# Optimization experiments

Hardware: AMD Instinct MI355X
Metric: run time of the kernel (lower is better)

The kernel has to match this reference:

```python
import jax, jax.numpy as jnp
import numpy as np

N = 100000
E = 1600000
D = 64
BETA = 1.0


def setup_inputs() -> dict:
    key = jax.random.key(0)
    ks = jax.random.split(key, 6)
    x = jax.random.normal(ks[0], (N, D), dtype=jnp.float32)
    edge_index = jax.random.randint(ks[1], (2, E), 0, N, dtype=jnp.int64)
    s = 1.0 / np.sqrt(D)
    Wm = jax.random.uniform(ks[2], (D, D), jnp.float32, -s, s)
    bm = jax.random.uniform(ks[3], (D,), jnp.float32, -s, s)
    Wr = jax.random.uniform(ks[4], (D, D), jnp.float32, -s, s)
    br = jax.random.uniform(ks[5], (D,), jnp.float32, -s, s)
    return {"x": x, "edge_index": edge_index, "Wm": Wm, "bm": bm, "Wr": Wr, "br": br}


def reference(x, edge_index, Wm, bm, Wr, br):
    row, col = edge_index[0], edge_index[1]
    # gather source features and apply message linear: [E, D]
    messages = x[row] @ Wm + bm
    scores = BETA * messages.mean(axis=-1)  # [E]
    # edge softmax over incoming edges of each destination node (col)
    seg_max = jax.ops.segment_max(scores, col, num_segments=N)  # [N]
    ex = jnp.exp(scores - seg_max[col])  # [E]
    seg_sum = jax.ops.segment_sum(ex, col, num_segments=N)  # [N]
    weights = ex / seg_sum[col]  # [E]
    # weighted scatter-add back to destinations
    out = jax.ops.segment_sum(messages * weights[:, None], col, num_segments=N)
    return out + (x @ Wr + br)
```

## Files before the change

kernel.cpp:

```cpp
#include <hip/hip_runtime.h>
#include <math.h>

#define N_NODES 100000
#define DIM 64
#define N_EDGES 1600000

#define NBF 1563
#define BK_NODES 64
#define CAP 1408

#define SC_CHUNK 8192
#define SC_BLOCKS ((N_EDGES + SC_CHUNK - 1) / SC_CHUNK)

#define GEMM_BLOCKS ((N_NODES / 16 + 15) / 16)
#define PH_BLOCKS (SC_BLOCKS + GEMM_BLOCKS)

typedef _Float16 half8 __attribute__((ext_vector_type(8)));
typedef _Float16 half4 __attribute__((ext_vector_type(4)));
typedef float f32x4 __attribute__((ext_vector_type(4)));

__global__ __launch_bounds__(1024) void k_phase(
        const float* __restrict__ x,
        const float* __restrict__ Wm, const float* __restrict__ bm,
        const float* __restrict__ Wr, const float* __restrict__ br,
        const int* __restrict__ row, const int* __restrict__ col,
        int* __restrict__ cursor, unsigned int* __restrict__ pairs,
        _Float16* __restrict__ Mh, float* __restrict__ es,
        float* __restrict__ out) {
    __shared__ int cnt[NBF];
    __shared__ int base_l[NBF];
    __shared__ int wsum[16];
    __shared__ int segtot;
    __shared__ unsigned int stage[SC_CHUNK];
    __shared__ unsigned short stage_bk[SC_CHUNK];

    const int t = threadIdx.x;
    const int lane = t & 63;
    const int wid = t >> 6;

    if (blockIdx.x < SC_BLOCKS) {
        const int start = blockIdx.x * SC_CHUNK;
        const int mEnd = min(N_EDGES, start + SC_CHUNK);

        for (int i = t; i < NBF; i += 1024) cnt[i] = 0;
        __syncthreads();

        int rr[8], cc[8], lr[8];
#pragma unroll
        for (int k = 0; k < 8; ++k) {
            const int idx = start + k * 1024 + t;
            if (idx < mEnd) {
                cc[k] = col[idx];
                rr[k] = row[idx];
                lr[k] = atomicAdd(&cnt[cc[k] >> 6], 1);
            }
        }
        __syncthreads();

        int segbase = 0;
        for (int s = 0; s < NBF; s += 1024) {
            const int i = s + t;
            const int v = (i < NBF) ? cnt[i] : 0;
            int inc = v;
#pragma unroll
            for (int o = 1; o < 64; o <<= 1) {
                const int u = __shfl_up(inc, o, 64);
                if (lane >= o) inc += u;
            }
            if (lane == 63) wsum[wid] = inc;
            __syncthreads();
            if (wid == 0) {
                const int wv = (lane < 16) ? wsum[lane] : 0;
                int winc = wv;
#pragma unroll
                for (int o = 1; o < 16; o <<= 1) {
                    const int u = __shfl_up(winc, o, 64);
                    if (lane >= o) winc += u;
                }
                if (lane < 16) wsum[lane] = winc - wv;
            }
            __syncthreads();
            const int excl = segbase + inc - v + wsum[wid];
            if (i < NBF) {
                base_l[i] = excl;
                if (v > 0) cnt[i] = atomicAdd(&cursor[i], v) - excl;
            }
            if (t == 1023) segtot = excl + v;
            __syncthreads();
            segbase = segtot;
        }

#pragma unroll
        for (int k = 0; k < 8; ++k) {
            const int idx = start + k * 1024 + t;
            if (idx < mEnd) {
                const int bk = cc[k] >> 6;
                const int slot = base_l[bk] + lr[k];
                stage[slot] = ((unsigned int)rr[k] << 6) | (unsigned int)(cc[k] & 63);
                stage_bk[slot] = (unsigned short)bk;
            }
        }
        __syncthreads();

        const int m = mEnd - start;
        for (int i = t; i < m; i += 1024) {
            const int bk = stage_bk[i];
            const int gslot = cnt[bk] + i;
            if (gslot < CAP) pairs[(size_t)bk * CAP + gslot] = stage[i];
        }
        return;
    }

    const int wave = (blockIdx.x - SC_BLOCKS) * 16 + wid;
    if (wave >= N_NODES / 16) return;
    const int quad = lane >> 4;
    const int l15 = lane & 15;
    const int row0 = wave * 16;

    half8 bfrag[8][2];
#pragma unroll
    for (int ct = 0; ct < 8; ++ct) {
        const float* W = (ct < 4) ? Wm : Wr;
        const int c = (ct & 3) * 16 + l15;
#pragma unroll
        for (int kc = 0; kc < 2; ++kc) {
            half8 f;
#pragma unroll
            for (int j = 0; j < 8; ++j)
                f[j] = (_Float16)W[(kc * 32 + quad * 8 + j) * DIM + c];
            bfrag[ct][kc] = f;
        }
    }

    half8 afrag[2];
#pragma unroll
    for (int kc = 0; kc < 2; ++kc) {
        const float* xp = x + (size_t)(row0 + l15) * DIM + kc * 32 + quad * 8;
        const float4 x0 = *(const float4*)xp;
        const float4 x1 = *(const float4*)(xp + 4);
        half8 f;
        f[0] = (_Float16)x0.x; f[1] = (_Float16)x0.y;
        f[2] = (_Float16)x0.z; f[3] = (_Float16)x0.w;
        f[4] = (_Float16)x1.x; f[5] = (_Float16)x1.y;
        f[6] = (_Float16)x1.z; f[7] = (_Float16)x1.w;
        afrag[kc] = f;
    }

    f32x4 acc[8];
#pragma unroll
    for (int ct = 0; ct < 8; ++ct) {
        f32x4 a = {0.f, 0.f, 0.f, 0.f};
        a = __builtin_amdgcn_mfma_f32_16x16x32_f16(afrag[0], bfrag[ct][0], a, 0, 0, 0);
        a = __builtin_amdgcn_mfma_f32_16x16x32_f16(afrag[1], bfrag[ct][1], a, 0, 0, 0);
        acc[ct] = a;
    }

    float rsum[4] = {0.f, 0.f, 0.f, 0.f};
#pragma unroll
    for (int ct = 0; ct < 8; ++ct) {
        const float bias = (ct < 4) ? bm[(ct & 3) * 16 + l15]
                                    : br[(ct & 3) * 16 + l15];
#pragma unroll
        for (int r = 0; r < 4; ++r) {
            const float v = acc[ct][r] + bias;
            const size_t idx = (size_t)(row0 + quad * 4 + r) * DIM + (ct & 3) * 16 + l15;
            if (ct < 4) {
                Mh[idx] = (_Float16)v;
                rsum[r] += v;
            } else {
                out[idx] = v;
            }
        }
    }
#pragma unroll
    for (int o = 1; o <= 8; o <<= 1) {
#pragma unroll
        for (int r = 0; r < 4; ++r) rsum[r] += __shfl_xor(rsum[r], o, 64);
    }
    if (l15 == 0) {
#pragma unroll
        for (int r = 0; r < 4; ++r)
            es[row0 + quad * 4 + r] = __expf(rsum[r] * (1.0f / DIM));
    }
}

__global__ __launch_bounds__(512) void k_bucket_gather(
        const unsigned int* __restrict__ pairs, const int* __restrict__ cursor,
        const float* __restrict__ es, const half4* __restrict__ Mh4,
        float4* __restrict__ out4) {
    __shared__ unsigned int sorted[CAP];
    __shared__ int cnt[BK_NODES];
    __shared__ int off[BK_NODES];
    const int b = blockIdx.x;
    const int t = threadIdx.x;
    const int lane = t & 63;
    const int wid = t >> 6;
    const int m = min(cursor[b], CAP);
    const size_t base = (size_t)b * CAP;

    if (t < BK_NODES) cnt[t] = 0;
    __syncthreads();

    unsigned int pk[3];
    int rk[3];
#pragma unroll
    for (int k = 0; k < 3; ++k) {
        const int i = k * 512 + t;
        if (i < m) {
            pk[k] = pairs[base + i];
            rk[k] = atomicAdd(&cnt[pk[k] & 63u], 1);
        }
    }
    __syncthreads();

    if (wid == 0) {
        const int v = cnt[lane];
        int inc = v;
#pragma unroll
        for (int o = 1; o < 64; o <<= 1) {
            const int u = __shfl_up(inc, o, 64);
            if (lane >= o) inc += u;
        }
        off[lane] = inc - v;
    }
    __syncthreads();

#pragma unroll
    for (int k = 0; k < 3; ++k) {
        const int i = k * 512 + t;
        if (i < m) sorted[off[pk[k] & 63u] + rk[k]] = pk[k];
    }
    __syncthreads();

    const int g = t >> 4;
    const int gl = t & 15;
    for (int c = g; c < BK_NODES; c += 32) {
        const int node = b * BK_NODES + c;
        if (node >= N_NODES) break;
        const int s0i = off[c];
        const int len = cnt[c];
        if (len == 0) continue;

        float a0x = 0.f, a0y = 0.f, a0z = 0.f, a0w = 0.f, l0 = 0.f;
        float a1x = 0.f, a1y = 0.f, a1z = 0.f, a1w = 0.f, l1 = 0.f;
        float a2x = 0.f, a2y = 0.f, a2z = 0.f, a2w = 0.f, l2 = 0.f;
        float a3x = 0.f, a3y = 0.f, a3z = 0.f, a3w = 0.f, l3 = 0.f;
        int j = 0;
        for (; j + 3 < len; j += 4) {
            const int s0 = (int)(sorted[s0i + j] >> 6);
            const int s1 = (int)(sorted[s0i + j + 1] >> 6);
            const int s2 = (int)(sorted[s0i + j + 2] >> 6);
            const int s3 = (int)(sorted[s0i + j + 3] >> 6);
            const float w0 = es[s0];
            const float w1 = es[s1];
            const float w2 = es[s2];
            const float w3 = es[s3];
            const half4 m0 = Mh4[(size_t)s0 * 16 + gl];
            const half4 m1 = Mh4[(size_t)s1 * 16 + gl];
            const half4 m2 = Mh4[(size_t)s2 * 16 + gl];
            const half4 m3 = Mh4[(size_t)s3 * 16 + gl];
            l0 += w0; l1 += w1; l2 += w2; l3 += w3;
            a0x = fmaf(w0, (float)m0[0], a0x); a0y = fmaf(w0, (float)m0[1], a0y);
            a0z = fmaf(w0, (float)m0[2], a0z); a0w = fmaf(w0, (float)m0[3], a0w);
            a1x = fmaf(w1, (float)m1[0], a1x); a1y = fmaf(w1, (float)m1[1], a1y);
            a1z = fmaf(w1, (float)m1[2], a1z); a1w = fmaf(w1, (float)m1[3], a1w);
            a2x = fmaf(w2, (float)m2[0], a2x); a2y = fmaf(w2, (float)m2[1], a2y);
            a2z = fmaf(w2, (float)m2[2], a2z); a2w = fmaf(w2, (float)m2[3], a2w);
            a3x = fmaf(w3, (float)m3[0], a3x); a3y = fmaf(w3, (float)m3[1], a3y);
            a3z = fmaf(w3, (float)m3[2], a3z); a3w = fmaf(w3, (float)m3[3], a3w);
        }
        for (; j < len; ++j) {
            const int s0 = (int)(sorted[s0i + j] >> 6);
            const float w0 = es[s0];
            const half4 m0 = Mh4[(size_t)s0 * 16 + gl];
            l0 += w0;
            a0x = fmaf(w0, (float)m0[0], a0x); a0y = fmaf(w0, (float)m0[1], a0y);
            a0z = fmaf(w0, (float)m0[2], a0z); a0w = fmaf(w0, (float)m0[3], a0w);
        }
        const float inv = 1.0f / (l0 + l1 + l2 + l3);
        float4 r = out4[(size_t)node * 16 + gl];
        r.x = fmaf(a0x + a1x + a2x + a3x, inv, r.x);
        r.y = fmaf(a0y + a1y + a2y + a3y, inv, r.y);
        r.z = fmaf(a0z + a1z + a2z + a3z, inv, r.z);
        r.w = fmaf(a0w + a1w + a2w + a3w, inv, r.w);
        out4[(size_t)node * 16 + gl] = r;
    }
}

extern "C" void kernel_launch(void* const* d_in, const int* in_sizes, int n_in,
                              void* d_out, int out_size, void* d_ws, size_t ws_size,
                              hipStream_t stream) {
    const float* x  = (const float*)d_in[0];
    const int*   ei = (const int*)d_in[1];
    const float* Wm = (const float*)d_in[2];
    const float* bm = (const float*)d_in[3];
    const float* Wr = (const float*)d_in[4];
    const float* br = (const float*)d_in[5];
    float* out = (float*)d_out;
    const int* row = ei;
    const int* col = ei + N_EDGES;

    char* ws = (char*)d_ws;
    _Float16* Mh    = (_Float16*)ws;     ws += (size_t)N_NODES * DIM * sizeof(_Float16);
    float* es       = (float*)ws;        ws += (size_t)N_NODES * sizeof(float);
    int* cursor     = (int*)ws;          ws += (size_t)2048 * sizeof(int);
    unsigned int* pairs = (unsigned int*)ws; ws += (size_t)NBF * CAP * sizeof(unsigned int);

    hipMemsetAsync(cursor, 0, NBF * sizeof(int), stream);

    k_phase<<<PH_BLOCKS, 1024, 0, stream>>>(x, Wm, bm, Wr, br, row, col,
                                            cursor, pairs, Mh, es, out);
    k_bucket_gather<<<NBF, 512, 0, stream>>>(pairs, cursor, es,
                                             (const half4*)Mh, (float4*)out);
}
```

Baseline: 153.4 us.

## Pre-transpose weights to fp16 in prep kernel and scatter edge pairs directly

Adds a single-block prep kernel that zeroes the bucket cursors (replacing the memset) and writes a transposed fp16 copy of Wm and Wr, so each GEMM wave loads its B fragments as vector half8 loads instead of strided scalar float loads with conversion. The scatter phase drops its block-local prefix scan and shared-memory staging. Each block now reserves global bucket offsets with one atomic per bucket and writes edge pairs straight to global memory. This cuts shared memory use and barriers, which may raise occupancy, but the global writes become less coalesced and an extra kernel launch is added.

```diff
diff --git a/kernel.cpp b/kernel.cpp
--- a/kernel.cpp
+++ b/kernel.cpp
@@ -19,20 +19,31 @@
 typedef _Float16 half4 __attribute__((ext_vector_type(4)));
 typedef float f32x4 __attribute__((ext_vector_type(4)));
 
+__global__ __launch_bounds__(1024) void k_prep(
+        const float* __restrict__ Wm, const float* __restrict__ Wr,
+        _Float16* __restrict__ Wt, int* __restrict__ cursor) {
+    const int t = threadIdx.x;
+    for (int i = t; i < NBF; i += 1024) cursor[i] = 0;
+#pragma unroll
+    for (int k = 0; k < 8; ++k) {
+        const int i = k * 1024 + t;
+        const int c = i >> 6;
+        const int kk = i & 63;
+        const float v = (c < 64) ? Wm[kk * 64 + c] : Wr[kk * 64 + (c - 64)];
+        Wt[i] = (_Float16)v;
+    }
+}
+
 __global__ __launch_bounds__(1024) void k_phase(
         const float* __restrict__ x,
-        const float* __restrict__ Wm, const float* __restrict__ bm,
-        const float* __restrict__ Wr, const float* __restrict__ br,
+        const _Float16* __restrict__ Wt,
+        const float* __restrict__ bm, const float* __restrict__ br,
         const int* __restrict__ row, const int* __restrict__ col,
         int* __restrict__ cursor, unsigned int* __restrict__ pairs,
         _Float16* __restrict__ Mh, float* __restrict__ es,
         float* __restrict__ out) {
     __shared__ int cnt[NBF];
-    __shared__ int base_l[NBF];
-    __shared__ int wsum[16];
-    __shared__ int segtot;
-    __shared__ unsigned int stage[SC_CHUNK];
-    __shared__ unsigned short stage_bk[SC_CHUNK];
+    __shared__ int basg[NBF];
 
     const int t = threadIdx.x;
     const int lane = t & 63;
@@ -57,56 +68,22 @@
         }
         __syncthreads();
 
-        int segbase = 0;
-        for (int s = 0; s < NBF; s += 1024) {
-            const int i = s + t;
-            const int v = (i < NBF) ? cnt[i] : 0;
-            int inc = v;
-#pragma unroll
-            for (int o = 1; o < 64; o <<= 1) {
-                const int u = __shfl_up(inc, o, 64);
-                if (lane >= o) inc += u;
-            }
-            if (lane == 63) wsum[wid] = inc;
-            __syncthreads();
-            if (wid == 0) {
-                const int wv = (lane < 16) ? wsum[lane] : 0;
-                int winc = wv;
-#pragma unroll
-                for (int o = 1; o < 16; o <<= 1) {
-                    const int u = __shfl_up(winc, o, 64);
-                    if (lane >= o) winc += u;
-                }
-                if (lane < 16) wsum[lane] = winc - wv;
-            }
-            __syncthreads();
-            const int excl = segbase + inc - v + wsum[wid];
-            if (i < NBF) {
-                base_l[i] = excl;
-                if (v > 0) cnt[i] = atomicAdd(&cursor[i], v) - excl;
-            }
-            if (t == 1023) segtot = excl + v;
-            __syncthreads();
-            segbase = segtot;
-        }
+        for (int i = t; i < NBF; i += 1024) {
+            const int v = cnt[i];
+            if (v > 0) basg[i] = atomicAdd(&cursor[i], v);
+        }
+        __syncthreads();
 
 #pragma unroll
         for (int k = 0; k < 8; ++k) {
             const int idx = start + k * 1024 + t;
             if (idx < mEnd) {
                 const int bk = cc[k] >> 6;
-                const int slot = base_l[bk] + lr[k];
-                stage[slot] = ((unsigned int)rr[k] << 6) | (unsigned int)(cc[k] & 63);
-                stage_bk[slot] = (unsigned short)bk;
+                const int gslot = basg[bk] + lr[k];
+                if (gslot < CAP)
+                    pairs[(size_t)bk * CAP + gslot] =
+                        ((unsigned int)rr[k] << 6) | (unsigned int)(cc[k] & 63);
             }
-        }
-        __syncthreads();
-
-        const int m = mEnd - start;
-        for (int i = t; i < m; i += 1024) {
-            const int bk = stage_bk[i];
-            const int gslot = cnt[bk] + i;
-            if (gslot < CAP) pairs[(size_t)bk * CAP + gslot] = stage[i];
         }
         return;
     }
@@ -117,19 +94,14 @@
     const int l15 = lane & 15;
     const int row0 = wave * 16;
 
+    const half8* __restrict__ Wt8 = (const half8*)Wt;
     half8 bfrag[8][2];
 #pragma unroll
     for (int ct = 0; ct < 8; ++ct) {
-        const float* W = (ct < 4) ? Wm : Wr;
-        const int c = (ct & 3) * 16 + l15;
-#pragma unroll
-        for (int kc = 0; kc < 2; ++kc) {
-            half8 f;
-#pragma unroll
-            for (int j = 0; j < 8; ++j)
-                f[j] = (_Float16)W[(kc * 32 + quad * 8 + j) * DIM + c];
-            bfrag[ct][kc] = f;
-        }
+        const int cidx = ((ct < 4) ? 0 : 64) + (ct & 3) * 16 + l15;
+#pragma unroll
+        for (int kc = 0; kc < 2; ++kc)
+            bfrag[ct][kc] = Wt8[cidx * 8 + kc * 4 + quad];
     }
 
     half8 afrag[2];
@@ -304,11 +276,11 @@
     _Float16* Mh    = (_Float16*)ws;     ws += (size_t)N_NODES * DIM * sizeof(_Float16);
     float* es       = (float*)ws;        ws += (size_t)N_NODES * sizeof(float);
     int* cursor     = (int*)ws;          ws += (size_t)2048 * sizeof(int);
+    _Float16* Wt    = (_Float16*)ws;     ws += (size_t)128 * 64 * sizeof(_Float16);
     unsigned int* pairs = (unsigned int*)ws; ws += (size_t)NBF * CAP * sizeof(unsigned int);
 
-    hipMemsetAsync(cursor, 0, NBF * sizeof(int), stream);
-
-    k_phase<<<PH_BLOCKS, 1024, 0, stream>>>(x, Wm, bm, Wr, br, row, col,
+    k_prep<<<1, 1024, 0, stream>>>(Wm, Wr, Wt, cursor);
+    k_phase<<<PH_BLOCKS, 1024, 0, stream>>>(x, Wt, bm, br, row, col,
                                             cursor, pairs, Mh, es, out);
     k_bucket_gather<<<NBF, 512, 0, stream>>>(pairs, cursor, es,
                                              (const half4*)Mh, (float4*)out);
```

After: 167.1 us. +8.9%, slower.

## Zero bucket cursors in-kernel behind a spin flag; gather with half8 per lane

Applied to the files above, without the earlier changes.

The host memset of the bucket cursors is removed. Block 0 of the phase kernel now zeroes them and publishes a magic flag, and every scatter block spin-waits on that flag before it takes its bucket cursor offsets. The gather kernel switches from 16 lanes per node with half4 loads to 8 lanes per node with half8 loads, so all 64 nodes of a bucket are handled at once without an inner node loop. Costs and risks: the flag is never reset, so on repeated calls the wait may no longer order the zeroing ahead of the cursor atomics. The spin also relies on block 0 being resident.

```diff
diff --git a/kernel.cpp b/kernel.cpp
--- a/kernel.cpp
+++ b/kernel.cpp
@@ -8,6 +8,9 @@
 #define NBF 1563
 #define BK_NODES 64
 #define CAP 1408
+
+#define CFLAG 2047
+#define CMAGIC 0x1357ACE9
 
 #define SC_CHUNK 8192
 #define SC_BLOCKS ((N_EDGES + SC_CHUNK - 1) / SC_CHUNK)
@@ -39,6 +42,15 @@
     const int wid = t >> 6;
 
     if (blockIdx.x < SC_BLOCKS) {
+        if (blockIdx.x == 0) {
+            for (int i = t; i < NBF; i += 1024) atomicExch(&cursor[i], 0);
+            __syncthreads();
+            if (t == 0) {
+                __threadfence();
+                atomicExch(&cursor[CFLAG], CMAGIC);
+            }
+        }
+
         const int start = blockIdx.x * SC_CHUNK;
         const int mEnd = min(N_EDGES, start + SC_CHUNK);
 
@@ -54,6 +66,11 @@
                 rr[k] = row[idx];
                 lr[k] = atomicAdd(&cnt[cc[k] >> 6], 1);
             }
+        }
+        __syncthreads();
+
+        if (t == 0) {
+            while (atomicAdd(&cursor[CFLAG], 0) != CMAGIC) {}
         }
         __syncthreads();
 
@@ -186,7 +203,7 @@
 
 __global__ __launch_bounds__(512) void k_bucket_gather(
         const unsigned int* __restrict__ pairs, const int* __restrict__ cursor,
-        const float* __restrict__ es, const half4* __restrict__ Mh4,
+        const float* __restrict__ es, const half8* __restrict__ Mh8,
         float4* __restrict__ out4) {
     __shared__ unsigned int sorted[CAP];
     __shared__ int cnt[BK_NODES];
@@ -232,59 +249,64 @@
     }
     __syncthreads();
 
-    const int g = t >> 4;
-    const int gl = t & 15;
-    for (int c = g; c < BK_NODES; c += 32) {
-        const int node = b * BK_NODES + c;
-        if (node >= N_NODES) break;
-        const int s0i = off[c];
-        const int len = cnt[c];
-        if (len == 0) continue;
-
-        float a0x = 0.f, a0y = 0.f, a0z = 0.f, a0w = 0.f, l0 = 0.f;
-        float a1x = 0.f, a1y = 0.f, a1z = 0.f, a1w = 0.f, l1 = 0.f;
-        float a2x = 0.f, a2y = 0.f, a2z = 0.f, a2w = 0.f, l2 = 0.f;
-        float a3x = 0.f, a3y = 0.f, a3z = 0.f, a3w = 0.f, l3 = 0.f;
-        int j = 0;
-        for (; j + 3 < len; j += 4) {
-            const int s0 = (int)(sorted[s0i + j] >> 6);
-            const int s1 = (int)(sorted[s0i + j + 1] >> 6);
-            const int s2 = (int)(sorted[s0i + j + 2] >> 6);
-            const int s3 = (int)(sorted[s0i + j + 3] >> 6);
-            const float w0 = es[s0];
-            const float w1 = es[s1];
-            const float w2 = es[s2];
-            const float w3 = es[s3];
-            const half4 m0 = Mh4[(size_t)s0 * 16 + gl];
-            const half4 m1 = Mh4[(size_t)s1 * 16 + gl];
-            const half4 m2 = Mh4[(size_t)s2 * 16 + gl];
-            const half4 m3 = Mh4[(size_t)s3 * 16 + gl];
-            l0 += w0; l1 += w1; l2 += w2; l3 += w3;
-            a0x = fmaf(w0, (float)m0[0], a0x); a0y = fmaf(w0, (float)m0[1], a0y);
-            a0z = fmaf(w0, (float)m0[2], a0z); a0w = fmaf(w0, (float)m0[3], a0w);
-            a1x = fmaf(w1, (float)m1[0], a1x); a1y = fmaf(w1, (float)m1[1], a1y);
-            a1z = fmaf(w1, (float)m1[2], a1z); a1w = fmaf(w1, (float)m1[3], a1w);
-            a2x = fmaf(w2, (float)m2[0], a2x); a2y = fmaf(w2, (float)m2[1], a2y);
-            a2z = fmaf(w2, (float)m2[2], a2z); a2w = fmaf(w2, (float)m2[3], a2w);
-            a3x = fmaf(w3, (float)m3[0], a3x); a3y = fmaf(w3, (float)m3[1], a3y);
-            a3z = fmaf(w3, (float)m3[2], a3z); a3w = fmaf(w3, (float)m3[3], a3w);
-        }
-        for (; j < len; ++j) {
-            const int s0 = (int)(sorted[s0i + j] >> 6);
-            const float w0 = es[s0];
-            const half4 m0 = Mh4[(size_t)s0 * 16 + gl];
-            l0 += w0;
-            a0x = fmaf(w0, (float)m0[0], a0x); a0y = fmaf(w0, (float)m0[1], a0y);
-            a0z = fmaf(w0, (float)m0[2], a0z); a0w = fmaf(w0, (float)m0[3], a0w);
-        }
-        const float inv = 1.0f / (l0 + l1 + l2 + l3);
-        float4 r = out4[(size_t)node * 16 + gl];
-        r.x = fmaf(a0x + a1x + a2x + a3x, inv, r.x);
-        r.y = fmaf(a0y + a1y + a2y + a3y, inv, r.y);
-        r.z = fmaf(a0z + a1z + a2z + a3z, inv, r.z);
-        r.w = fmaf(a0w + a1w + a2w + a3w, inv, r.w);
-        out4[(size_t)node * 16 + gl] = r;
-    }
+    const int g = t >> 3;
+    const int gl = t & 7;
+    const int node = b * BK_NODES + g;
+    if (node >= N_NODES) return;
+    const int s0i = off[g];
+    const int len = cnt[g];
+    if (len == 0) return;
+
+    float a0[8], a1[8], a2[8], a3[8];
+    float l0 = 0.f, l1 = 0.f, l2 = 0.f, l3 = 0.f;
+#pragma unroll
+    for (int d = 0; d < 8; ++d) { a0[d] = 0.f; a1[d] = 0.f; a2[d] = 0.f; a3[d] = 0.f; }
+
+    int j = 0;
+    for (; j + 3 < len; j += 4) {
+        const int s0 = (int)(sorted[s0i + j] >> 6);
+        const int s1 = (int)(sorted[s0i + j + 1] >> 6);
+        const int s2 = (int)(sorted[s0i + j + 2] >> 6);
+        const int s3 = (int)(sorted[s0i + j + 3] >> 6);
+        const float w0 = es[s0];
+        const float w1 = es[s1];
+        const float w2 = es[s2];
+        const float w3 = es[s3];
+        const half8 m0 = Mh8[(size_t)s0 * 8 + gl];
+        const half8 m1 = Mh8[(size_t)s1 * 8 + gl];
+        const half8 m2 = Mh8[(size_t)s2 * 8 + gl];
+        const half8 m3 = Mh8[(size_t)s3 * 8 + gl];
+        l0 += w0; l1 += w1; l2 += w2; l3 += w3;
+#pragma unroll
+        for (int d = 0; d < 8; ++d) {
+            a0[d] = fmaf(w0, (float)m0[d], a0[d]);
+            a1[d] = fmaf(w1, (float)m1[d], a1[d]);
+            a2[d] = fmaf(w2, (float)m2[d], a2[d]);
+            a3[d] = fmaf(w3, (float)m3[d], a3[d]);
+        }
+    }
+    for (; j < len; ++j) {
+        const int s0 = (int)(sorted[s0i + j] >> 6);
+        const float w0 = es[s0];
+        const half8 m0 = Mh8[(size_t)s0 * 8 + gl];
+        l0 += w0;
+#pragma unroll
+        for (int d = 0; d < 8; ++d) a0[d] = fmaf(w0, (float)m0[d], a0[d]);
+    }
+
+    const float inv = 1.0f / (l0 + l1 + l2 + l3);
+    float4 r0 = out4[(size_t)node * 16 + gl * 2];
+    float4 r1 = out4[(size_t)node * 16 + gl * 2 + 1];
+    r0.x = fmaf(a0[0] + a1[0] + a2[0] + a3[0], inv, r0.x);
+    r0.y = fmaf(a0[1] + a1[1] + a2[1] + a3[1], inv, r0.y);
+    r0.z = fmaf(a0[2] + a1[2] + a2[2] + a3[2], inv, r0.z);
+    r0.w = fmaf(a0[3] + a1[3] + a2[3] + a3[3], inv, r0.w);
+    r1.x = fmaf(a0[4] + a1[4] + a2[4] + a3[4], inv, r1.x);
+    r1.y = fmaf(a0[5] + a1[5] + a2[5] + a3[5], inv, r1.y);
+    r1.z = fmaf(a0[6] + a1[6] + a2[6] + a3[6], inv, r1.z);
+    r1.w = fmaf(a0[7] + a1[7] + a2[7] + a3[7], inv, r1.w);
+    out4[(size_t)node * 16 + gl * 2] = r0;
+    out4[(size_t)node * 16 + gl * 2 + 1] = r1;
 }
 
 extern "C" void kernel_launch(void* const* d_in, const int* in_sizes, int n_in,
@@ -306,10 +328,8 @@
     int* cursor     = (int*)ws;          ws += (size_t)2048 * sizeof(int);
     unsigned int* pairs = (unsigned int*)ws; ws += (size_t)NBF * CAP * sizeof(unsigned int);
 
-    hipMemsetAsync(cursor, 0, NBF * sizeof(int), stream);
-
     k_phase<<<PH_BLOCKS, 1024, 0, stream>>>(x, Wm, bm, Wr, br, row, col,
                                             cursor, pairs, Mh, es, out);
     k_bucket_gather<<<NBF, 512, 0, stream>>>(pairs, cursor, es,
-                                             (const half4*)Mh, (float4*)out);
+                                             (const half8*)Mh, (float4*)out);
 }
```

After: 154.4 us. About the same (+0.7%).
